# Performance work log

Measured on AMD Instinct MI355X. Metric: run time of the kernel, lower is better.

The kernel has to match this reference:

```python
import jax, jax.numpy as jnp
import numpy as np

B, T, D, C = 16, 1500, 768, 1024

def setup_inputs() -> dict:
    key = jax.random.key(0)
    k1, k2 = jax.random.split(key)
    embed = jax.random.normal(k1, (B, T, D), dtype=jnp.float32)
    cluster_centers = jax.random.normal(k2, (C, D), dtype=jnp.float32)
    return {"embed": embed, "cluster_centers": cluster_centers}

def reference(embed, cluster_centers):
    # Faithful to: dists = -torch.cdist(embed, centers, p=2); clusters = dists.argmax(-1)
    # Euclidean distance via ||e||^2 - 2 e.c + ||c||^2 (GEMM-friendly form).
    e_sq = jnp.sum(embed * embed, axis=-1, keepdims=True)            # (b, t, 1)
    c_sq = jnp.sum(cluster_centers * cluster_centers, axis=-1)       # (c,)
    cross = jnp.einsum('btd,cd->btc', embed, cluster_centers)        # (b, t, c)
    d2 = jnp.maximum(e_sq - 2.0 * cross + c_sq, 0.0)
    dists = -jnp.sqrt(d2)                                            # negative L2 distance
    clusters = jnp.argmax(dists, axis=-1)                            # (b, t) int
    return clusters
```

## Files before the change

### kernel.cpp

```cpp
#include <hip/hip_runtime.h>
#include <cstdint>
#include <cstddef>

#define MROWS 24000
#define NCOLS 1024
#define KDIM  768
#define MT 188
#define KT 48
#define NT 4

typedef _Float16 f16x8  __attribute__((ext_vector_type(8)));
typedef float    f32x16 __attribute__((ext_vector_type(16)));

typedef __attribute__((address_space(1))) void as1_void;
typedef __attribute__((address_space(3))) void as3_void;

#define A_BYTES   (188ull*48*8192)
#define B_OFF     A_BYTES
#define B_BYTES   (4ull*48*16384)
#define CH_OFF    (A_BYTES + B_BYTES)
#define PART_OFF  (CH_OFF + 4096)
#define WS_NEED   (PART_OFF + 24064ull*4*8)

__global__ void k_tile_A(const float* __restrict__ E, _Float16* __restrict__ Aw) {
  int bid = blockIdx.x;
  int mt = bid / 48, kt = bid % 48;
  int t = threadIdx.x;
  int r = t >> 1, p = t & 1;
  int row = mt * 128 + r;
  __shared__ _Float16 lh[2][128][8];
  __shared__ _Float16 ll[2][128][8];
  float x[8];
  if (row < MROWS) {
    const float4* s4 = (const float4*)(E + (size_t)row * KDIM + kt * 16 + p * 8);
    float4 v0 = s4[0], v1 = s4[1];
    x[0]=v0.x; x[1]=v0.y; x[2]=v0.z; x[3]=v0.w; x[4]=v1.x; x[5]=v1.y; x[6]=v1.z; x[7]=v1.w;
  } else {
#pragma unroll
    for (int e = 0; e < 8; ++e) x[e] = 0.f;
  }
#pragma unroll
  for (int e = 0; e < 8; ++e) {
    _Float16 h = (_Float16)x[e];
    lh[p][r][e] = h;
    ll[p][r][e] = (_Float16)(x[e] - (float)h);
  }
  __syncthreads();
  const uint4* sh = (const uint4*)&lh[0][0][0];
  const uint4* sl = (const uint4*)&ll[0][0][0];
  uint4* dst = (uint4*)(Aw + (size_t)bid * 4096);
  dst[t]       = sh[t];
  dst[256 + t] = sl[t];
}

__global__ void k_tile_B(const float* __restrict__ C, _Float16* __restrict__ Bw) {
  int bid = blockIdx.x;
  int nt = bid / 48, kt = bid % 48;
  int t = threadIdx.x;
  int c = t >> 1, p = t & 1;
  __shared__ _Float16 lh[2][256][8];
  __shared__ _Float16 ll[2][256][8];
  const float4* s4 = (const float4*)(C + (size_t)(nt * 256 + c) * KDIM + kt * 16 + p * 8);
  float4 v0 = s4[0], v1 = s4[1];
  float x[8] = {v0.x, v0.y, v0.z, v0.w, v1.x, v1.y, v1.z, v1.w};
#pragma unroll
  for (int e = 0; e < 8; ++e) {
    _Float16 h = (_Float16)x[e];
    lh[p][c][e] = h;
    ll[p][c][e] = (_Float16)(x[e] - (float)h);
  }
  __syncthreads();
  const uint4* sh = (const uint4*)&lh[0][0][0];
  const uint4* sl = (const uint4*)&ll[0][0][0];
  uint4* dst = (uint4*)(Bw + (size_t)bid * 8192);
  dst[t]       = sh[t];
  dst[512 + t] = sl[t];
}

__global__ void k_chalf(const float* __restrict__ C, float* __restrict__ ch) {
  int c = blockIdx.x, t = threadIdx.x;
  const float* src = C + (size_t)c * KDIM;
  float sq = 0.f;
#pragma unroll
  for (int i = 0; i < 3; ++i) {
    float x = src[t + i * 256];
    sq = fmaf(x, x, sq);
  }
#pragma unroll
  for (int m = 1; m < 64; m <<= 1) sq += __shfl_xor(sq, m, 64);
  __shared__ float part[4];
  if ((t & 63) == 0) part[t >> 6] = sq;
  __syncthreads();
  if (t == 0) ch[c] = 0.5f * ((part[0] + part[1]) + (part[2] + part[3]));
}

#define MFMA16(a, b, c) __builtin_amdgcn_mfma_f32_32x32x16_f16((a), (b), (c), 0, 0, 0)

__global__ __launch_bounds__(512, 4) void k_gemm(
    const _Float16* __restrict__ Aw, const _Float16* __restrict__ Bw,
    const float* __restrict__ ch, uint2* __restrict__ part) {
  __shared__ __align__(16) char smem[3][24576];
  __shared__ float red_v[4][128];
  __shared__ int   red_i[4][128];

  const int bid0 = blockIdx.x;
  const int swz = (bid0 & 7) * 94 + (bid0 >> 3);
  const int nt = swz / MT, mt = swz % MT;

  const int tid = threadIdx.x, lane = tid & 63, wid = tid >> 6;
  const int wm = wid >> 2, wn = wid & 3;
  const int lo5 = lane & 31, p = lane >> 5;

  const char* Ab = (const char*)Aw + (size_t)mt * (48 * 8192);
  const char* Bb = (const char*)Bw + (size_t)nt * (48 * 16384);

  auto stageA = [&](char* sb, int kt) {
    __builtin_amdgcn_global_load_lds((as1_void*)(Ab + kt * 8192 + tid * 16),
                                     (as3_void*)(sb + tid * 16), 16, 0, 0);
  };
  auto stageB0 = [&](char* sb, int kt) {
    __builtin_amdgcn_global_load_lds((as1_void*)(Bb + kt * 16384 + tid * 16),
                                     (as3_void*)(sb + 8192 + tid * 16), 16, 0, 0);
  };
  auto stageB1 = [&](char* sb, int kt) {
    __builtin_amdgcn_global_load_lds((as1_void*)(Bb + kt * 16384 + 8192 + tid * 16),
                                     (as3_void*)(sb + 16384 + tid * 16), 16, 0, 0);
  };

  f32x16 acc[2][2] = {};
  const int offA = p * 2048 + (wm * 64 + lo5) * 16;
  const int offB = p * 4096 + (wn * 64 + lo5) * 16;

  char* rb = smem[0];
  char* nb = smem[1];
  char* wb = smem[2];

  stageA(smem[0], 0); stageB0(smem[0], 0); stageB1(smem[0], 0);
  stageA(smem[1], 1); stageB0(smem[1], 1); stageB1(smem[1], 1);

  for (int j = 0; j < KT; ++j) {
    if (j < KT - 1) asm volatile("s_waitcnt vmcnt(3)" ::: "memory");
    else            asm volatile("s_waitcnt vmcnt(0)" ::: "memory");
    __builtin_amdgcn_s_barrier();

    f16x8 ah0 = *(const f16x8*)(rb + offA);
    f16x8 ah1 = *(const f16x8*)(rb + offA + 512);
    f16x8 al0 = *(const f16x8*)(rb + 4096 + offA);
    f16x8 al1 = *(const f16x8*)(rb + 4096 + offA + 512);
    f16x8 bh0 = *(const f16x8*)(rb + 8192 + offB);
    f16x8 bl0 = *(const f16x8*)(rb + 16384 + offB);
    if (j + 2 < KT) { stageA(wb, j + 2); stageB0(wb, j + 2); }
    __builtin_amdgcn_s_barrier();
    __builtin_amdgcn_s_setprio(1);
    acc[0][0] = MFMA16(ah0, bh0, acc[0][0]);
    acc[0][0] = MFMA16(ah0, bl0, acc[0][0]);
    acc[0][0] = MFMA16(al0, bh0, acc[0][0]);
    acc[1][0] = MFMA16(ah1, bh0, acc[1][0]);
    acc[1][0] = MFMA16(ah1, bl0, acc[1][0]);
    acc[1][0] = MFMA16(al1, bh0, acc[1][0]);
    __builtin_amdgcn_s_setprio(0);
    __builtin_amdgcn_s_barrier();

    f16x8 bh1 = *(const f16x8*)(rb + 8192 + offB + 512);
    f16x8 bl1 = *(const f16x8*)(rb + 16384 + offB + 512);
    if (j + 2 < KT) stageB1(wb, j + 2);
    __builtin_amdgcn_s_barrier();
    __builtin_amdgcn_s_setprio(1);
    acc[0][1] = MFMA16(ah0, bh1, acc[0][1]);
    acc[0][1] = MFMA16(ah0, bl1, acc[0][1]);
    acc[0][1] = MFMA16(al0, bh1, acc[0][1]);
    acc[1][1] = MFMA16(ah1, bh1, acc[1][1]);
    acc[1][1] = MFMA16(ah1, bl1, acc[1][1]);
    acc[1][1] = MFMA16(al1, bh1, acc[1][1]);
    __builtin_amdgcn_s_setprio(0);

    char* t = rb; rb = nb; nb = wb; wb = t;
  }

  int c0 = nt * 256 + wn * 64 + lo5;
  int c1 = c0 + 32;
  float ch0 = ch[c0];
  float ch1 = ch[c1];
#pragma unroll
  for (int mi = 0; mi < 2; ++mi)
#pragma unroll
    for (int q = 0; q < 16; ++q) {
      float s0 = acc[mi][0][q] - ch0;
      float s1 = acc[mi][1][q] - ch1;
      float v = s0; int ix = c0;
      if (s1 > v) { v = s1; ix = c1; }
#pragma unroll
      for (int m = 1; m <= 16; m <<= 1) {
        float ov = __shfl_xor(v, m, 64);
        int   oi = __shfl_xor(ix, m, 64);
        if (ov > v || (ov == v && oi < ix)) { v = ov; ix = oi; }
      }
      if (lo5 == 0) {
        int rr = (q & 3) + ((q >> 2) << 3) + (p << 2);
        int rloc = wm * 64 + mi * 32 + rr;
        red_v[wn][rloc] = v;
        red_i[wn][rloc] = ix;
      }
    }
  __syncthreads();
  if (tid < 128) {
    float v = red_v[0][tid];
    int ix = red_i[0][tid];
#pragma unroll
    for (int w = 1; w < 4; ++w) {
      float ov = red_v[w][tid];
      int oi = red_i[w][tid];
      if (ov > v) { v = ov; ix = oi; }
    }
    int rowg = mt * 128 + tid;
    part[rowg * 4 + nt] = uint2{ __float_as_uint(v), (unsigned)ix };
  }
}

__global__ void k_merge(const uint2* __restrict__ part, int* __restrict__ out) {
  int r = blockIdx.x * 256 + threadIdx.x;
  if (r >= MROWS) return;
  uint2 b0 = part[r * 4];
  float bvv = __uint_as_float(b0.x);
  int bii = (int)b0.y;
#pragma unroll
  for (int j = 1; j < 4; ++j) {
    uint2 pj = part[r * 4 + j];
    float v = __uint_as_float(pj.x);
    if (v > bvv) { bvv = v; bii = (int)pj.y; }
  }
  out[r] = bii;
}

__global__ void k_naive(const float* __restrict__ E, const float* __restrict__ C,
                        int* __restrict__ out) {
  int row = blockIdx.x * 4 + (threadIdx.x >> 6);
  int lane = threadIdx.x & 63;
  const float* e = E + (size_t)row * KDIM;
  float bvv = -3.4e38f;
  int bii = 0;
  for (int c = 0; c < NCOLS; ++c) {
    const float* cc = C + (size_t)c * KDIM;
    float dot = 0.f, csq = 0.f;
    for (int d = lane; d < KDIM; d += 64) {
      float cv = cc[d];
      dot = fmaf(e[d], cv, dot);
      csq = fmaf(cv, cv, csq);
    }
#pragma unroll
    for (int m = 1; m < 64; m <<= 1) {
      dot += __shfl_xor(dot, m, 64);
      csq += __shfl_xor(csq, m, 64);
    }
    float s = dot - 0.5f * csq;
    if (s > bvv) { bvv = s; bii = c; }
  }
  if (lane == 0) out[row] = bii;
}

extern "C" void kernel_launch(void* const* d_in, const int* in_sizes, int n_in,
                              void* d_out, int out_size, void* d_ws, size_t ws_size,
                              hipStream_t stream) {
  const float* embed   = (const float*)d_in[0];
  const float* centers = (const float*)d_in[1];
  int* out = (int*)d_out;

  if (ws_size >= WS_NEED) {
    char* w = (char*)d_ws;
    _Float16* Aw = (_Float16*)w;
    _Float16* Bw = (_Float16*)(w + B_OFF);
    float*    ch = (float*)(w + CH_OFF);
    uint2*  partb = (uint2*)(w + PART_OFF);
    k_tile_A<<<188 * 48, 256, 0, stream>>>(embed, Aw);
    k_tile_B<<<4 * 48, 512, 0, stream>>>(centers, Bw);
    k_chalf<<<1024, 256, 0, stream>>>(centers, ch);
    k_gemm<<<752, 512, 0, stream>>>(Aw, Bw, ch, partb);
    k_merge<<<94, 256, 0, stream>>>(partb, out);
  } else {
    k_naive<<<6000, 256, 0, stream>>>(embed, centers, out);
  }
}
```

Before: 171.0 us.

## Load B operand directly into registers and shrink LDS to A-only ring

The B (cluster-center) fragments are now read straight from global memory into registers one k-tile ahead, instead of being staged through LDS. Only the A tile still goes through a three-buffer LDS ring, which cuts shared memory per block from about 72KB to about 24KB. The per-k-tile barriers drop from three to one, and the loop is unrolled by three with fixed buffer roles. The smaller LDS footprint and fewer barriers could allow more resident blocks and less synchronization. The cost is redundant global or cache reads of B across waves, and B latency that the single-tile register prefetch may not hide, because the in-order vmcnt wait ties it to the A prefetch.

```diff
diff --git a/kernel.cpp b/kernel.cpp
--- a/kernel.cpp
+++ b/kernel.cpp
@@ -99,7 +99,7 @@
 __global__ __launch_bounds__(512, 4) void k_gemm(
     const _Float16* __restrict__ Aw, const _Float16* __restrict__ Bw,
     const float* __restrict__ ch, uint2* __restrict__ part) {
-  __shared__ __align__(16) char smem[3][24576];
+  __shared__ __align__(16) char smem[3][8192];
   __shared__ float red_v[4][128];
   __shared__ int   red_i[4][128];
 
@@ -118,39 +118,31 @@
     __builtin_amdgcn_global_load_lds((as1_void*)(Ab + kt * 8192 + tid * 16),
                                      (as3_void*)(sb + tid * 16), 16, 0, 0);
   };
-  auto stageB0 = [&](char* sb, int kt) {
-    __builtin_amdgcn_global_load_lds((as1_void*)(Bb + kt * 16384 + tid * 16),
-                                     (as3_void*)(sb + 8192 + tid * 16), 16, 0, 0);
-  };
-  auto stageB1 = [&](char* sb, int kt) {
-    __builtin_amdgcn_global_load_lds((as1_void*)(Bb + kt * 16384 + 8192 + tid * 16),
-                                     (as3_void*)(sb + 16384 + tid * 16), 16, 0, 0);
-  };
 
   f32x16 acc[2][2] = {};
   const int offA = p * 2048 + (wm * 64 + lo5) * 16;
   const int offB = p * 4096 + (wn * 64 + lo5) * 16;
 
-  char* rb = smem[0];
-  char* nb = smem[1];
-  char* wb = smem[2];
-
-  stageA(smem[0], 0); stageB0(smem[0], 0); stageB1(smem[0], 0);
-  stageA(smem[1], 1); stageB0(smem[1], 1); stageB1(smem[1], 1);
-
-  for (int j = 0; j < KT; ++j) {
-    if (j < KT - 1) asm volatile("s_waitcnt vmcnt(3)" ::: "memory");
-    else            asm volatile("s_waitcnt vmcnt(0)" ::: "memory");
+  f16x8 bh0, bh1, bl0, bl1;
+  auto loadB = [&](int kt) {
+    const char* gb = Bb + (size_t)kt * 16384;
+    bh0 = *(const f16x8*)(gb + offB);
+    bh1 = *(const f16x8*)(gb + offB + 512);
+    bl0 = *(const f16x8*)(gb + 8192 + offB);
+    bl1 = *(const f16x8*)(gb + 8192 + offB + 512);
+  };
+
+  stageA(smem[0], 0);
+  stageA(smem[1], 1);
+  loadB(0);
+
+  auto ktile = [&](const char* rb, char* wb, int j) {
+    asm volatile("s_waitcnt vmcnt(5)" ::: "memory");
     __builtin_amdgcn_s_barrier();
-
     f16x8 ah0 = *(const f16x8*)(rb + offA);
     f16x8 ah1 = *(const f16x8*)(rb + offA + 512);
     f16x8 al0 = *(const f16x8*)(rb + 4096 + offA);
     f16x8 al1 = *(const f16x8*)(rb + 4096 + offA + 512);
-    f16x8 bh0 = *(const f16x8*)(rb + 8192 + offB);
-    f16x8 bl0 = *(const f16x8*)(rb + 16384 + offB);
-    if (j + 2 < KT) { stageA(wb, j + 2); stageB0(wb, j + 2); }
-    __builtin_amdgcn_s_barrier();
     __builtin_amdgcn_s_setprio(1);
     acc[0][0] = MFMA16(ah0, bh0, acc[0][0]);
     acc[0][0] = MFMA16(ah0, bl0, acc[0][0]);
@@ -158,14 +150,6 @@
     acc[1][0] = MFMA16(ah1, bh0, acc[1][0]);
     acc[1][0] = MFMA16(ah1, bl0, acc[1][0]);
     acc[1][0] = MFMA16(al1, bh0, acc[1][0]);
-    __builtin_amdgcn_s_setprio(0);
-    __builtin_amdgcn_s_barrier();
-
-    f16x8 bh1 = *(const f16x8*)(rb + 8192 + offB + 512);
-    f16x8 bl1 = *(const f16x8*)(rb + 16384 + offB + 512);
-    if (j + 2 < KT) stageB1(wb, j + 2);
-    __builtin_amdgcn_s_barrier();
-    __builtin_amdgcn_s_setprio(1);
     acc[0][1] = MFMA16(ah0, bh1, acc[0][1]);
     acc[0][1] = MFMA16(ah0, bl1, acc[0][1]);
     acc[0][1] = MFMA16(al0, bh1, acc[0][1]);
@@ -173,8 +157,14 @@
     acc[1][1] = MFMA16(ah1, bl1, acc[1][1]);
     acc[1][1] = MFMA16(al1, bh1, acc[1][1]);
     __builtin_amdgcn_s_setprio(0);
-
-    char* t = rb; rb = nb; nb = wb; wb = t;
+    if (j + 2 < KT) stageA(wb, j + 2);
+    if (j + 1 < KT) loadB(j + 1);
+  };
+
+  for (int j = 0; j < KT; j += 3) {
+    ktile(smem[0], smem[2], j);
+    ktile(smem[1], smem[0], j + 1);
+    ktile(smem[2], smem[1], j + 2);
   }
 
   int c0 = nt * 256 + wn * 64 + lo5;
```

New measurement: 176.5 us. 3.2% more time.
